# Kernel optimization log

Measured on AMD Instinct MI355X. Metric: run time of the kernel, lower is better.

## Reference

```python
import jax, jax.numpy as jnp
import numpy as np

SRC_LEN, TRG_LEN, BATCH, HID_DIM, ATT_DIM = 256, 256, 32, 512, 128


def setup_inputs() -> dict:
    key = jax.random.key(0)
    k1, k2, k3, k4, k5, k6 = jax.random.split(key, 6)
    dec_out = jax.random.normal(k1, (TRG_LEN, BATCH, HID_DIM), dtype=jnp.float32)
    enc_outs = jax.random.normal(k2, (SRC_LEN, BATCH, HID_DIM), dtype=jnp.float32)
    # Linear weights (scaled like kaiming-ish init so tanh isn't saturated)
    W_s = jax.random.normal(k3, (ATT_DIM, HID_DIM), dtype=jnp.float32) / np.sqrt(HID_DIM)
    W_t = jax.random.normal(k4, (ATT_DIM, HID_DIM), dtype=jnp.float32) / np.sqrt(HID_DIM)
    b_t = jax.random.normal(k5, (ATT_DIM,), dtype=jnp.float32) * 0.01
    # v_a ~ U(-0.05, 0.05), shape (att_dim, 1) as in the torch module
    v_a = jax.random.uniform(k6, (ATT_DIM, 1), dtype=jnp.float32, minval=-0.05, maxval=0.05)
    return {"dec_out": dec_out, "enc_outs": enc_outs, "W_s": W_s, "W_t": W_t, "b_t": b_t, "v_a": v_a}


def reference(dec_out, enc_outs, W_s, W_t, b_t, v_a):
    # enc projection: (src, batch, hid) -> (src, batch, att)
    enc_att = jnp.einsum('sbh,ah->sba', enc_outs, W_s)
    # dec projection (with bias): (trg, batch, hid) -> (trg, batch, att)
    dec_att = jnp.einsum('tbh,ah->tba', dec_out, W_t) + b_t
    # broadcast-add + tanh: (src, trg, batch, att), then reduce with v_a
    dec_enc = jnp.tanh(enc_att[:, None, :, :] + dec_att[None, :, :, :])
    scores = jnp.einsum('stba,a->tbs', dec_enc, v_a[:, 0])  # (trg, batch, src)
    return scores
```

## Files before the change

kernel.cpp:

```cpp
#include <hip/hip_runtime.h>

#define SRC_LEN 256
#define TRG_LEN 256
#define BATCH   32
#define HID     512
#define ATT     128
#define CSCALE  2.885390081777927f

typedef float  f32x4  __attribute__((ext_vector_type(4)));
typedef short  bf16x8 __attribute__((ext_vector_type(8)));

__device__ inline unsigned short bfr(float x) {
    unsigned u = __builtin_bit_cast(unsigned, x);
    return (unsigned short)((u + 0x7fffu + ((u >> 16) & 1u)) >> 16);
}
__device__ inline unsigned pk2(float a, float b) {
    return (unsigned)bfr(a) | ((unsigned)bfr(b) << 16);
}

__global__ __launch_bounds__(512) void proj_mfma(
    const float* __restrict__ dec_out, const float* __restrict__ enc_outs,
    const float* __restrict__ W_s, const float* __restrict__ W_t,
    const float* __restrict__ b_t,
    float* __restrict__ encE, float* __restrict__ decD)
{
    __shared__ __align__(16) char smem[49152];
    char* aLb = smem;
    char* bLb = smem + 16384;

    const int tid   = threadIdx.x;
    const int blk   = blockIdx.x;
    const bool isDec = blk >= 128;
    const int bb    = blk & 31;
    const int r0    = ((isDec ? blk - 128 : blk) >> 5) * 64;
    const float* __restrict__ in = isDec ? dec_out : enc_outs;
    const float* __restrict__ W  = isDec ? W_t : W_s;

    const int lane   = tid & 63;
    const int w      = tid >> 6;
    const int woff_m = (w & 3) * 16;
    const int woff_n = (w >> 2) * 64;
    const int q      = lane >> 4;
    const int l15    = lane & 15;
    const int l7     = lane & 7;

    const int srow = tid >> 4;
    const int skc  = tid & 15;
    const int sg   = skc >> 1, shalf = skc & 1;
    const float* aGp = in + ((size_t)(r0 + srow) * BATCH + bb) * HID + skc * 4;
    const float* wGp = W + (size_t)srow * HID + skc * 4;

    float4 aR[2];
    float4 wR[4];

    f32x4 acc[4];
    #pragma unroll
    for (int ni = 0; ni < 4; ++ni) acc[ni] = (f32x4)0.0f;

    #define LOADG(c)                                                          \
        {                                                                     \
            _Pragma("unroll")                                                 \
            for (int it = 0; it < 2; ++it)                                    \
                aR[it] = *(const float4*)(aGp + (size_t)it * 32 * BATCH * HID \
                                          + (c) * 64);                        \
            _Pragma("unroll")                                                 \
            for (int it = 0; it < 4; ++it)                                    \
                wR[it] = *(const float4*)(wGp + (size_t)it * 32 * HID         \
                                          + (c) * 64);                        \
        }

    #define STORES(buf)                                                      \
        {                                                                    \
            char* ab = aLb + (buf) * 8192;                                   \
            _Pragma("unroll")                                                \
            for (int it = 0; it < 2; ++it) {                                 \
                const int i = srow + it * 32;                                \
                uint2 u;                                                     \
                u.x = pk2(aR[it].x, aR[it].y);                               \
                u.y = pk2(aR[it].z, aR[it].w);                               \
                *(uint2*)(ab + i * 128 + ((sg ^ (i & 7)) << 4)               \
                          + shalf * 8) = u;                                  \
            }                                                                \
            char* bp = bLb + (buf) * 16384;                                  \
            _Pragma("unroll")                                                \
            for (int it = 0; it < 4; ++it) {                                 \
                const int rw = srow + it * 32;                               \
                uint2 u;                                                     \
                u.x = pk2(wR[it].x, wR[it].y);                               \
                u.y = pk2(wR[it].z, wR[it].w);                               \
                *(uint2*)(bp + rw * 128 + ((sg ^ (rw & 7)) << 4)             \
                          + shalf * 8) = u;                                  \
            }                                                                \
        }

    LOADG(0);
    STORES(0);
    __syncthreads();

    for (int c = 0; c < 8; ++c) {
        if (c < 7) LOADG(c + 1);
        const char* ab = aLb + (c & 1) * 8192;
        const char* bp = bLb + (c & 1) * 16384;
        #pragma unroll
        for (int s = 0; s < 2; ++s) {
            const int sw = ((s * 4 + q) ^ l7) * 16;
            bf16x8 af = *(const bf16x8*)(ab + (woff_m + l15) * 128 + sw);
            bf16x8 bfv[4];
            #pragma unroll
            for (int ni = 0; ni < 4; ++ni)
                bfv[ni] = *(const bf16x8*)(bp + (woff_n + ni * 16 + l15) * 128 + sw);
            #pragma unroll
            for (int ni = 0; ni < 4; ++ni)
                acc[ni] = __builtin_amdgcn_mfma_f32_16x16x32_bf16(
                    af, bfv[ni], acc[ni], 0, 0, 0);
        }
        if (c < 7) STORES((c + 1) & 1);
        __syncthreads();
    }

    if (!isDec) {
        float* T = (float*)smem;
        #pragma unroll
        for (int ni = 0; ni < 4; ++ni)
            #pragma unroll
            for (int r = 0; r < 4; ++r) {
                const int ml = woff_m + q * 4 + r;
                const int nl = woff_n + ni * 16 + l15;
                T[ml * 132 + nl] = __builtin_amdgcn_exp2f(-CSCALE * acc[ni][r]);
            }
        __syncthreads();
        {
            const int m  = tid & 63;
            const int g0 = tid >> 6;
            #pragma unroll
            for (int p = 0; p < 4; ++p) {
                const int gq = g0 + p * 8;
                float4 v = *(const float4*)(T + m * 132 + gq * 4);
                *(float4*)(encE + (((size_t)bb * 32 + gq) * SRC_LEN + r0 + m) * 4) = v;
            }
        }
    } else {
        float bt[4];
        #pragma unroll
        for (int ni = 0; ni < 4; ++ni) bt[ni] = b_t[woff_n + ni * 16 + l15];
        #pragma unroll
        for (int ni = 0; ni < 4; ++ni)
            #pragma unroll
            for (int r = 0; r < 4; ++r) {
                const int ml = woff_m + q * 4 + r;
                const int nl = woff_n + ni * 16 + l15;
                decD[((size_t)(r0 + ml) * BATCH + bb) * ATT + nl] =
                    __builtin_amdgcn_exp2f(CSCALE * (acc[ni][r] + bt[ni]));
            }
    }
    #undef LOADG
    #undef STORES
}

__global__ __launch_bounds__(256) void score_kernel(
    const float* __restrict__ encE, const float* __restrict__ decD,
    const float* __restrict__ v_a, float* __restrict__ out)
{
    __shared__ float dS[4 * ATT];
    __shared__ float vS[ATT];
    __shared__ float sumvS;

    const int tid = threadIdx.x;
    const int t0  = blockIdx.x * 4;
    const int b   = blockIdx.y;

    if (tid < 128) {
        const int tt = tid >> 5, a4 = (tid & 31) * 4;
        *(float4*)(dS + tt * ATT + a4) =
            *(const float4*)(decD + ((size_t)(t0 + tt) * BATCH + b) * ATT + a4);
    } else if (tid < 160) {
        const int l = tid - 128;
        *(float4*)(vS + l * 4) = *(const float4*)(v_a + l * 4);
    }
    __syncthreads();
    if (tid < 64) {
        float x = vS[tid] + vS[tid + 64];
        #pragma unroll
        for (int o = 32; o > 0; o >>= 1) x += __shfl_down(x, o);
        if (tid == 0) sumvS = x;
    }
    __syncthreads();

    float acc0 = 0.f, acc1 = 0.f, acc2 = 0.f, acc3 = 0.f;
    const float* __restrict__ ep = encE + ((size_t)b * 32 * SRC_LEN + tid) * 4;

    #pragma unroll
    for (int g = 0; g < 32; ++g) {
        const float4 E  = *(const float4*)(ep + (size_t)g * SRC_LEN * 4);
        const float4 vv = *(const float4*)(vS + g * 4);
        const float n0 = vv.x * E.x, n1 = vv.y * E.y;
        const float n2 = vv.z * E.z, n3 = vv.w * E.w;

        #define TSTEP(ACC, DBASE)                                          \
        {                                                                  \
            const float4 d = *(const float4*)(DBASE + g * 4);              \
            const float x0 = E.x + d.x, x1 = E.y + d.y;                    \
            const float x2 = E.z + d.z, x3 = E.w + d.w;                    \
            const float a01 = x0 * x1, a23 = x2 * x3;                      \
            const float den = a01 * a23;                                   \
            const float m01 = fmaf(n0, x1, n1 * x0);                       \
            const float m23 = fmaf(n2, x3, n3 * x2);                       \
            const float num = fmaf(m01, a23, m23 * a01);                   \
            ACC = fmaf(num, __builtin_amdgcn_rcpf(den), ACC);              \
        }
        TSTEP(acc0, dS + 0 * ATT)
        TSTEP(acc1, dS + 1 * ATT)
        TSTEP(acc2, dS + 2 * ATT)
        TSTEP(acc3, dS + 3 * ATT)
        #undef TSTEP
    }

    const float sv = sumvS;
    out[((size_t)(t0 + 0) * BATCH + b) * SRC_LEN + tid] = sv - 2.0f * acc0;
    out[((size_t)(t0 + 1) * BATCH + b) * SRC_LEN + tid] = sv - 2.0f * acc1;
    out[((size_t)(t0 + 2) * BATCH + b) * SRC_LEN + tid] = sv - 2.0f * acc2;
    out[((size_t)(t0 + 3) * BATCH + b) * SRC_LEN + tid] = sv - 2.0f * acc3;
}

extern "C" void kernel_launch(void* const* d_in, const int* in_sizes, int n_in,
                              void* d_out, int out_size, void* d_ws, size_t ws_size,
                              hipStream_t stream) {
    const float* dec_out  = (const float*)d_in[0];
    const float* enc_outs = (const float*)d_in[1];
    const float* W_s      = (const float*)d_in[2];
    const float* W_t      = (const float*)d_in[3];
    const float* b_t      = (const float*)d_in[4];
    const float* v_a      = (const float*)d_in[5];
    float* out = (float*)d_out;

    float* encE = (float*)d_ws;
    float* decD = encE + (size_t)BATCH * ATT * SRC_LEN;

    proj_mfma<<<256, 512, 0, stream>>>(dec_out, enc_outs, W_s, W_t, b_t, encE, decD);

    dim3 g3(TRG_LEN / 4, BATCH);
    score_kernel<<<g3, 256, 0, stream>>>(encE, decD, v_a, out);
}
```

Before: 115.9 us.

## Shrink projection tiles to 16 rows and launch 1024 smaller blocks

The projection GEMM tile drops from 64 rows by 512 threads to 16 rows by 256 threads, and the grid grows from 256 to 1024 blocks. The goal is to fill all CUs on the device (256 blocks underfill MI355X) and allow several blocks per CU. The cost is that each block reloads the full 128-row weight chunk for only 16 activation rows, so weight traffic and LDS conversion work per output rise about fourfold.

```diff
diff --git a/kernel.cpp b/kernel.cpp
--- a/kernel.cpp
+++ b/kernel.cpp
@@ -18,31 +18,30 @@
     return (unsigned)bfr(a) | ((unsigned)bfr(b) << 16);
 }
 
-__global__ __launch_bounds__(512) void proj_mfma(
+__global__ __launch_bounds__(256, 4) void proj_mfma(
     const float* __restrict__ dec_out, const float* __restrict__ enc_outs,
     const float* __restrict__ W_s, const float* __restrict__ W_t,
     const float* __restrict__ b_t,
     float* __restrict__ encE, float* __restrict__ decD)
 {
-    __shared__ __align__(16) char smem[49152];
+    __shared__ __align__(16) char smem[36864];
     char* aLb = smem;
-    char* bLb = smem + 16384;
+    char* bLb = smem + 4096;
 
     const int tid   = threadIdx.x;
     const int blk   = blockIdx.x;
-    const bool isDec = blk >= 128;
-    const int bb    = blk & 31;
-    const int r0    = ((isDec ? blk - 128 : blk) >> 5) * 64;
+    const bool isDec = blk >= 512;
+    const int idx   = blk & 511;
+    const int bb    = idx & 31;
+    const int r0    = (idx >> 5) * 16;
     const float* __restrict__ in = isDec ? dec_out : enc_outs;
     const float* __restrict__ W  = isDec ? W_t : W_s;
 
-    const int lane   = tid & 63;
-    const int w      = tid >> 6;
-    const int woff_m = (w & 3) * 16;
-    const int woff_n = (w >> 2) * 64;
-    const int q      = lane >> 4;
-    const int l15    = lane & 15;
-    const int l7     = lane & 7;
+    const int lane = tid & 63;
+    const int w    = tid >> 6;
+    const int q    = lane >> 4;
+    const int l15  = lane & 15;
+    const int l7   = lane & 7;
 
     const int srow = tid >> 4;
     const int skc  = tid & 15;
@@ -50,41 +49,36 @@
     const float* aGp = in + ((size_t)(r0 + srow) * BATCH + bb) * HID + skc * 4;
     const float* wGp = W + (size_t)srow * HID + skc * 4;
 
-    float4 aR[2];
-    float4 wR[4];
-
-    f32x4 acc[4];
-    #pragma unroll
-    for (int ni = 0; ni < 4; ++ni) acc[ni] = (f32x4)0.0f;
+    float4 aR;
+    float4 wR[8];
+
+    f32x4 acc[2];
+    acc[0] = (f32x4)0.0f;
+    acc[1] = (f32x4)0.0f;
 
     #define LOADG(c)                                                          \
         {                                                                     \
+            aR = *(const float4*)(aGp + (c) * 64);                            \
             _Pragma("unroll")                                                 \
-            for (int it = 0; it < 2; ++it)                                    \
-                aR[it] = *(const float4*)(aGp + (size_t)it * 32 * BATCH * HID \
-                                          + (c) * 64);                        \
-            _Pragma("unroll")                                                 \
-            for (int it = 0; it < 4; ++it)                                    \
-                wR[it] = *(const float4*)(wGp + (size_t)it * 32 * HID         \
+            for (int it = 0; it < 8; ++it)                                    \
+                wR[it] = *(const float4*)(wGp + (size_t)it * 16 * HID         \
                                           + (c) * 64);                        \
         }
 
     #define STORES(buf)                                                      \
         {                                                                    \
-            char* ab = aLb + (buf) * 8192;                                   \
-            _Pragma("unroll")                                                \
-            for (int it = 0; it < 2; ++it) {                                 \
-                const int i = srow + it * 32;                                \
+            char* ab = aLb + (buf) * 2048;                                   \
+            {                                                                \
                 uint2 u;                                                     \
-                u.x = pk2(aR[it].x, aR[it].y);                               \
-                u.y = pk2(aR[it].z, aR[it].w);                               \
-                *(uint2*)(ab + i * 128 + ((sg ^ (i & 7)) << 4)               \
+                u.x = pk2(aR.x, aR.y);                                       \
+                u.y = pk2(aR.z, aR.w);                                       \
+                *(uint2*)(ab + srow * 128 + ((sg ^ (srow & 7)) << 4)         \
                           + shalf * 8) = u;                                  \
             }                                                                \
             char* bp = bLb + (buf) * 16384;                                  \
             _Pragma("unroll")                                                \
-            for (int it = 0; it < 4; ++it) {                                 \
-                const int rw = srow + it * 32;                               \
+            for (int it = 0; it < 8; ++it) {                                 \
+                const int rw = srow + it * 16;                               \
                 uint2 u;                                                     \
                 u.x = pk2(wR[it].x, wR[it].y);                               \
                 u.y = pk2(wR[it].z, wR[it].w);                               \
@@ -99,20 +93,16 @@
 
     for (int c = 0; c < 8; ++c) {
         if (c < 7) LOADG(c + 1);
-        const char* ab = aLb + (c & 1) * 8192;
+        const char* ab = aLb + (c & 1) * 2048;
         const char* bp = bLb + (c & 1) * 16384;
         #pragma unroll
         for (int s = 0; s < 2; ++s) {
             const int sw = ((s * 4 + q) ^ l7) * 16;
-            bf16x8 af = *(const bf16x8*)(ab + (woff_m + l15) * 128 + sw);
-            bf16x8 bfv[4];
-            #pragma unroll
-            for (int ni = 0; ni < 4; ++ni)
-                bfv[ni] = *(const bf16x8*)(bp + (woff_n + ni * 16 + l15) * 128 + sw);
-            #pragma unroll
-            for (int ni = 0; ni < 4; ++ni)
-                acc[ni] = __builtin_amdgcn_mfma_f32_16x16x32_bf16(
-                    af, bfv[ni], acc[ni], 0, 0, 0);
+            bf16x8 af = *(const bf16x8*)(ab + l15 * 128 + sw);
+            bf16x8 b0 = *(const bf16x8*)(bp + (w * 32 + l15) * 128 + sw);
+            bf16x8 b1 = *(const bf16x8*)(bp + (w * 32 + 16 + l15) * 128 + sw);
+            acc[0] = __builtin_amdgcn_mfma_f32_16x16x32_bf16(af, b0, acc[0], 0, 0, 0);
+            acc[1] = __builtin_amdgcn_mfma_f32_16x16x32_bf16(af, b1, acc[1], 0, 0, 0);
         }
         if (c < 7) STORES((c + 1) & 1);
         __syncthreads();
@@ -121,37 +111,35 @@
     if (!isDec) {
         float* T = (float*)smem;
         #pragma unroll
-        for (int ni = 0; ni < 4; ++ni)
+        for (int ni = 0; ni < 2; ++ni)
             #pragma unroll
             for (int r = 0; r < 4; ++r) {
-                const int ml = woff_m + q * 4 + r;
-                const int nl = woff_n + ni * 16 + l15;
+                const int ml = q * 4 + r;
+                const int nl = w * 32 + ni * 16 + l15;
                 T[ml * 132 + nl] = __builtin_amdgcn_exp2f(-CSCALE * acc[ni][r]);
             }
         __syncthreads();
         {
-            const int m  = tid & 63;
-            const int g0 = tid >> 6;
+            const int m  = tid & 15;
+            const int g0 = tid >> 4;
             #pragma unroll
-            for (int p = 0; p < 4; ++p) {
-                const int gq = g0 + p * 8;
+            for (int p = 0; p < 2; ++p) {
+                const int gq = g0 + p * 16;
                 float4 v = *(const float4*)(T + m * 132 + gq * 4);
                 *(float4*)(encE + (((size_t)bb * 32 + gq) * SRC_LEN + r0 + m) * 4) = v;
             }
         }
     } else {
-        float bt[4];
-        #pragma unroll
-        for (int ni = 0; ni < 4; ++ni) bt[ni] = b_t[woff_n + ni * 16 + l15];
-        #pragma unroll
-        for (int ni = 0; ni < 4; ++ni)
-            #pragma unroll
-            for (int r = 0; r < 4; ++r) {
-                const int ml = woff_m + q * 4 + r;
-                const int nl = woff_n + ni * 16 + l15;
-                decD[((size_t)(r0 + ml) * BATCH + bb) * ATT + nl] =
-                    __builtin_amdgcn_exp2f(CSCALE * (acc[ni][r] + bt[ni]));
-            }
+        float bt0 = b_t[w * 32 + l15];
+        float bt1 = b_t[w * 32 + 16 + l15];
+        #pragma unroll
+        for (int r = 0; r < 4; ++r) {
+            const int t = r0 + q * 4 + r;
+            decD[((size_t)t * BATCH + bb) * ATT + w * 32 + l15] =
+                __builtin_amdgcn_exp2f(CSCALE * (acc[0][r] + bt0));
+            decD[((size_t)t * BATCH + bb) * ATT + w * 32 + 16 + l15] =
+                __builtin_amdgcn_exp2f(CSCALE * (acc[1][r] + bt1));
+        }
     }
     #undef LOADG
     #undef STORES
@@ -236,7 +224,7 @@
     float* encE = (float*)d_ws;
     float* decD = encE + (size_t)BATCH * ATT * SRC_LEN;
 
-    proj_mfma<<<256, 512, 0, stream>>>(dec_out, enc_outs, W_s, W_t, b_t, encE, decD);
+    proj_mfma<<<1024, 256, 0, stream>>>(dec_out, enc_outs, W_s, W_t, b_t, encE, decD);
 
     dim3 g3(TRG_LEN / 4, BATCH);
     score_kernel<<<g3, 256, 0, stream>>>(encE, decD, v_a, out);
```

Measured after the change: 122.5 us. 5.7% more time.

## Stream decoder terms via scalar loads with v-premultiplied interleaved layout

Applied to the files above, without the earlier changes.

The projection kernel now writes decoder exp terms in a per-(batch, t-quad, group) interleaved layout that also holds v_a times D. The score kernel drops its LDS staging, barriers and v_a reduction, and instead streams these uniform values through double-buffered s_load_dwordx16 into scalar registers, so they become SGPR operands of the VALU math. Because the premultiplied v*D now feeds the numerator, the sign of the final combination flips. This removes LDS reads and syncs from the inner loop. In exchange it relies on hand-written inline asm waitcnt handling and uses a fair number of SGPRs.

```diff
diff --git a/kernel.cpp b/kernel.cpp
--- a/kernel.cpp
+++ b/kernel.cpp
@@ -8,6 +8,7 @@
 #define CSCALE  2.885390081777927f
 
 typedef float  f32x4  __attribute__((ext_vector_type(4)));
+typedef float  f32x16 __attribute__((ext_vector_type(16)));
 typedef short  bf16x8 __attribute__((ext_vector_type(8)));
 
 __device__ inline unsigned short bfr(float x) {
@@ -21,8 +22,8 @@
 __global__ __launch_bounds__(512) void proj_mfma(
     const float* __restrict__ dec_out, const float* __restrict__ enc_outs,
     const float* __restrict__ W_s, const float* __restrict__ W_t,
-    const float* __restrict__ b_t,
-    float* __restrict__ encE, float* __restrict__ decD)
+    const float* __restrict__ b_t, const float* __restrict__ v_a,
+    float* __restrict__ encE, float* __restrict__ decR)
 {
     __shared__ __align__(16) char smem[49152];
     char* aLb = smem;
@@ -140,86 +141,101 @@
             }
         }
     } else {
-        float bt[4];
-        #pragma unroll
-        for (int ni = 0; ni < 4; ++ni) bt[ni] = b_t[woff_n + ni * 16 + l15];
-        #pragma unroll
-        for (int ni = 0; ni < 4; ++ni)
+        float bt[4], vA[4];
+        #pragma unroll
+        for (int ni = 0; ni < 4; ++ni) {
+            bt[ni] = b_t[woff_n + ni * 16 + l15];
+            vA[ni] = v_a[woff_n + ni * 16 + l15];
+        }
+        const int tqB = (r0 + woff_m) >> 2;
+        const int i   = l15 & 3;
+        #pragma unroll
+        for (int ni = 0; ni < 4; ++ni) {
+            const int g = ((woff_n + ni * 16) >> 2) + (l15 >> 2);
             #pragma unroll
             for (int r = 0; r < 4; ++r) {
-                const int ml = woff_m + q * 4 + r;
-                const int nl = woff_n + ni * 16 + l15;
-                decD[((size_t)(r0 + ml) * BATCH + bb) * ATT + nl] =
-                    __builtin_amdgcn_exp2f(CSCALE * (acc[ni][r] + bt[ni]));
+                const float Dv = __builtin_amdgcn_exp2f(CSCALE * (acc[ni][r] + bt[ni]));
+                float* p = decR + (((size_t)bb * 64 + (tqB + q)) * 32 + g) * 32 + r * 4 + i;
+                p[0]  = Dv;
+                p[16] = vA[ni] * Dv;
             }
+        }
     }
     #undef LOADG
     #undef STORES
 }
 
 __global__ __launch_bounds__(256) void score_kernel(
-    const float* __restrict__ encE, const float* __restrict__ decD,
+    const float* __restrict__ encE, const float* __restrict__ decR,
     const float* __restrict__ v_a, float* __restrict__ out)
 {
-    __shared__ float dS[4 * ATT];
-    __shared__ float vS[ATT];
-    __shared__ float sumvS;
-
     const int tid = threadIdx.x;
-    const int t0  = blockIdx.x * 4;
+    const int tq  = blockIdx.x;
     const int b   = blockIdx.y;
 
-    if (tid < 128) {
-        const int tt = tid >> 5, a4 = (tid & 31) * 4;
-        *(float4*)(dS + tt * ATT + a4) =
-            *(const float4*)(decD + ((size_t)(t0 + tt) * BATCH + b) * ATT + a4);
-    } else if (tid < 160) {
-        const int l = tid - 128;
-        *(float4*)(vS + l * 4) = *(const float4*)(v_a + l * 4);
-    }
-    __syncthreads();
-    if (tid < 64) {
-        float x = vS[tid] + vS[tid + 64];
-        #pragma unroll
-        for (int o = 32; o > 0; o >>= 1) x += __shfl_down(x, o);
-        if (tid == 0) sumvS = x;
-    }
-    __syncthreads();
-
-    float acc0 = 0.f, acc1 = 0.f, acc2 = 0.f, acc3 = 0.f;
-    const float* __restrict__ ep = encE + ((size_t)b * 32 * SRC_LEN + tid) * 4;
-
+    float sv = 0.f;
     #pragma unroll
     for (int g = 0; g < 32; ++g) {
+        const float4 v4 = *(const float4*)(v_a + g * 4);
+        sv += (v4.x + v4.y) + (v4.z + v4.w);
+    }
+
+    const float* __restrict__ ep = encE + ((size_t)b * 32 * SRC_LEN + tid) * 4;
+    const float* rp = decR + ((size_t)b * 64 + tq) * 32 * 32;
+
+    f32x16 d0, n0, d1, n1;
+    asm volatile("s_load_dwordx16 %0, %2, 0x0\n\t"
+                 "s_load_dwordx16 %1, %2, 0x40"
+                 : "=s"(d0), "=s"(n0) : "s"(rp));
+
+    float acc0 = 0.f, acc1 = 0.f, acc2 = 0.f, acc3 = 0.f;
+
+    #pragma unroll
+    for (int g = 0; g < 32; ++g) {
+        if (g & 1) { asm volatile("s_waitcnt lgkmcnt(0)" : "+s"(d1), "+s"(n1)); }
+        else       { asm volatile("s_waitcnt lgkmcnt(0)" : "+s"(d0), "+s"(n0)); }
+        if (g < 31) {
+            const float* np = rp + (size_t)(g + 1) * 32;
+            if (g & 1)
+                asm volatile("s_load_dwordx16 %0, %2, 0x0\n\t"
+                             "s_load_dwordx16 %1, %2, 0x40"
+                             : "=s"(d0), "=s"(n0) : "s"(np));
+            else
+                asm volatile("s_load_dwordx16 %0, %2, 0x0\n\t"
+                             "s_load_dwordx16 %1, %2, 0x40"
+                             : "=s"(d1), "=s"(n1) : "s"(np));
+        }
+        const f32x16 dd = (g & 1) ? d1 : d0;
+        const f32x16 nn = (g & 1) ? n1 : n0;
         const float4 E  = *(const float4*)(ep + (size_t)g * SRC_LEN * 4);
-        const float4 vv = *(const float4*)(vS + g * 4);
-        const float n0 = vv.x * E.x, n1 = vv.y * E.y;
-        const float n2 = vv.z * E.z, n3 = vv.w * E.w;
-
-        #define TSTEP(ACC, DBASE)                                          \
-        {                                                                  \
-            const float4 d = *(const float4*)(DBASE + g * 4);              \
-            const float x0 = E.x + d.x, x1 = E.y + d.y;                    \
-            const float x2 = E.z + d.z, x3 = E.w + d.w;                    \
-            const float a01 = x0 * x1, a23 = x2 * x3;                      \
-            const float den = a01 * a23;                                   \
-            const float m01 = fmaf(n0, x1, n1 * x0);                       \
-            const float m23 = fmaf(n2, x3, n3 * x2);                       \
-            const float num = fmaf(m01, a23, m23 * a01);                   \
-            ACC = fmaf(num, __builtin_amdgcn_rcpf(den), ACC);              \
-        }
-        TSTEP(acc0, dS + 0 * ATT)
-        TSTEP(acc1, dS + 1 * ATT)
-        TSTEP(acc2, dS + 2 * ATT)
-        TSTEP(acc3, dS + 3 * ATT)
+
+        #define TSTEP(ACC, T)                                                 \
+        {                                                                     \
+            const float x0 = E.x + dd[(T) * 4 + 0];                           \
+            const float x1 = E.y + dd[(T) * 4 + 1];                           \
+            const float x2 = E.z + dd[(T) * 4 + 2];                           \
+            const float x3 = E.w + dd[(T) * 4 + 3];                           \
+            const float a01 = x0 * x1, a23 = x2 * x3;                         \
+            const float den = a01 * a23;                                      \
+            const float m01 = fmaf(nn[(T) * 4 + 0], x1,                       \
+                                   nn[(T) * 4 + 1] * x0);                     \
+            const float m23 = fmaf(nn[(T) * 4 + 2], x3,                       \
+                                   nn[(T) * 4 + 3] * x2);                     \
+            const float num = fmaf(m01, a23, m23 * a01);                      \
+            ACC = fmaf(num, __builtin_amdgcn_rcpf(den), ACC);                 \
+        }
+        TSTEP(acc0, 0)
+        TSTEP(acc1, 1)
+        TSTEP(acc2, 2)
+        TSTEP(acc3, 3)
         #undef TSTEP
     }
 
-    const float sv = sumvS;
-    out[((size_t)(t0 + 0) * BATCH + b) * SRC_LEN + tid] = sv - 2.0f * acc0;
-    out[((size_t)(t0 + 1) * BATCH + b) * SRC_LEN + tid] = sv - 2.0f * acc1;
-    out[((size_t)(t0 + 2) * BATCH + b) * SRC_LEN + tid] = sv - 2.0f * acc2;
-    out[((size_t)(t0 + 3) * BATCH + b) * SRC_LEN + tid] = sv - 2.0f * acc3;
+    const int t0 = tq * 4;
+    out[((size_t)(t0 + 0) * BATCH + b) * SRC_LEN + tid] = 2.0f * acc0 - sv;
+    out[((size_t)(t0 + 1) * BATCH + b) * SRC_LEN + tid] = 2.0f * acc1 - sv;
+    out[((size_t)(t0 + 2) * BATCH + b) * SRC_LEN + tid] = 2.0f * acc2 - sv;
+    out[((size_t)(t0 + 3) * BATCH + b) * SRC_LEN + tid] = 2.0f * acc3 - sv;
 }
 
 extern "C" void kernel_launch(void* const* d_in, const int* in_sizes, int n_in,
@@ -234,10 +250,10 @@
     float* out = (float*)d_out;
 
     float* encE = (float*)d_ws;
-    float* decD = encE + (size_t)BATCH * ATT * SRC_LEN;
-
-    proj_mfma<<<256, 512, 0, stream>>>(dec_out, enc_outs, W_s, W_t, b_t, encE, decD);
+    float* decR = encE + (size_t)BATCH * ATT * SRC_LEN;
+
+    proj_mfma<<<256, 512, 0, stream>>>(dec_out, enc_outs, W_s, W_t, b_t, v_a, encE, decR);
 
     dim3 g3(TRG_LEN / 4, BATCH);
-    score_kernel<<<g3, 256, 0, stream>>>(encE, decD, v_a, out);
-}
+    score_kernel<<<g3, 256, 0, stream>>>(encE, decR, v_a, out);
+}
```

New measurement: 210.7 us. 1.82x slower.
